# Kernel tuning notes

Measured on AMD Instinct MI355X. Metric: run time of the kernel, lower is better.

## Reference

```python
import jax, jax.numpy as jnp
import numpy as np
from jax import lax

ALPHA = 1.5
N_ITER = 50  # entmax bisect default
GAIN = 1.414


def _p(z):
    # gp_inv(clamp(z,0), alpha) = z_+^(1/(alpha-1)) = z_+^2 for alpha=1.5
    zc = jnp.clip(z, 0.0, None)
    return zc * zc


def entmax15(X):
    """alpha-entmax (alpha=1.5) along last dim via bisection (entmax lib algorithm)."""
    d = X.shape[-1]
    Xs = X * (ALPHA - 1.0)
    mx = jnp.max(Xs, axis=-1, keepdims=True)
    tau_lo = mx - 1.0                       # gp(1, alpha) = 1
    tau_hi = mx - (1.0 / d) ** (ALPHA - 1.0)  # gp(1/d, alpha)
    f_lo = jnp.sum(_p(Xs - tau_lo), axis=-1, keepdims=True) - 1.0

    def body(i, carry):
        tau_lo, dm = carry
        dm = dm * 0.5
        tau_m = tau_lo + dm
        f_m = jnp.sum(_p(Xs - tau_m), axis=-1, keepdims=True) - 1.0
        tau_lo = jnp.where(f_m * f_lo >= 0.0, tau_m, tau_lo)
        return (tau_lo, dm)

    tau_lo, _ = lax.fori_loop(0, N_ITER, body, (tau_lo, tau_hi - tau_lo))
    p = _p(Xs - tau_lo)
    return p / jnp.sum(p, axis=-1, keepdims=True)  # ensure_sum_one=True


def _xavier(key, shape):
    std = GAIN * (2.0 / (shape[0] + shape[1])) ** 0.5
    a = (3.0 ** 0.5) * std
    return jax.random.uniform(key, shape, minval=-a, maxval=a, dtype=jnp.float32)


def setup_inputs() -> dict:
    B, F, E, N = 2048, 64, 256, 64  # batch, nfield, nemb, ncross
    key = jax.random.key(0)
    k1, k2, k3, k4 = jax.random.split(key, 4)
    return {
        "x": jax.random.normal(k1, (B, F, E), dtype=jnp.float32),
        "bilinear_w": _xavier(k2, (E, E)),
        "query": _xavier(k3, (N, E)),
        "value": _xavier(k4, (N, F)),
    }


def reference(x, bilinear_w, query, value):
    # x: [B,F,E]; bilinear_w: [E,E]; query: [N,E]; value: [N,F]
    scale = x.shape[-1] ** -0.5
    k = jnp.einsum('bfe,de->bfd', x, bilinear_w)        # [B,F,E]
    att_gate = jnp.einsum('bfd,nd->bnf', k, query) * scale  # [B,N,F]
    sparse_gate = entmax15(att_gate)                     # entmax over F
    attn_weight = sparse_gate * value[None]              # [B,N,F]
    return jnp.exp(jnp.einsum('bfe,bnf->bne', x, attn_weight))  # [B,N,E]
```

## Files before the change

### kernel.cpp

```cpp
#include <hip/hip_runtime.h>
#include <hip/hip_bf16.h>

typedef __attribute__((ext_vector_type(8))) short bf16x8;
typedef __attribute__((ext_vector_type(4))) float f32x4;

__device__ __forceinline__ unsigned int pk2(float a, float b) {
  union { __hip_bfloat162 h; unsigned int u; } cv;
  cv.h = __float22bfloat162_rn(make_float2(a, b));
  return cv.u;
}
__device__ __forceinline__ unsigned short f2bf(float f) {
  unsigned int u = __float_as_uint(f);
  u += 0x7FFFu + ((u >> 16) & 1u);
  return (unsigned short)(u >> 16);
}

__device__ __forceinline__ float dpp_xor1(float v) {
  return __int_as_float(__builtin_amdgcn_update_dpp(
      0, __float_as_int(v), 0xB1, 0xF, 0xF, true));
}
__device__ __forceinline__ float dpp_xor2(float v) {
  return __int_as_float(__builtin_amdgcn_update_dpp(
      0, __float_as_int(v), 0x4E, 0xF, 0xF, true));
}

__global__ void __launch_bounds__(256) qw_kernel(const float* __restrict__ q,
                                                 const float* __restrict__ W,
                                                 unsigned short* __restrict__ qw) {
  int n = blockIdx.x, e = threadIdx.x;
  float acc = 0.f;
  #pragma unroll 8
  for (int d = 0; d < 256; ++d) acc = fmaf(q[n * 256 + d], W[d * 256 + e], acc);
  qw[n * 256 + e] = f2bf(acc * 0.0625f);
}

__global__ void __launch_bounds__(512, 6) cross_main(
    const float* __restrict__ x, const float* __restrict__ value,
    const unsigned short* __restrict__ qw, float* __restrict__ out) {

  __shared__ __align__(16) unsigned short lds_x[64 * 268];
  __shared__ __align__(16) unsigned char  lds_pool[64 * 68 * 4];

  float* lds_att = (float*)lds_pool;
  unsigned short* lds_aw = (unsigned short*)lds_pool;

  const int t = threadIdx.x;
  const int b = blockIdx.x;
  const int l = t & 63;
  const int w = t >> 6;
  const int l15 = l & 15, l4 = l >> 4;

  {
    const float4* xg = (const float4*)(x + (size_t)b * 16384);
    #pragma unroll
    for (int it = 0; it < 4; ++it) {
      int u = it * 512 + t;
      float4 v0 = xg[2 * u], v1 = xg[2 * u + 1];
      int f = u >> 5, c8 = u & 31;
      char* dst = (char*)lds_x + f * 536 + c8 * 16;
      *(uint2*)dst       = make_uint2(pk2(v0.x, v0.y), pk2(v0.z, v0.w));
      *(uint2*)(dst + 8) = make_uint2(pk2(v1.x, v1.y), pk2(v1.z, v1.w));
    }
  }
  __syncthreads();

  {
    int nt = w >> 1, ft0 = (w & 1) * 2;
    f32x4 acc0 = {0.f, 0.f, 0.f, 0.f}, acc1 = {0.f, 0.f, 0.f, 0.f};
    const unsigned short* qa = qw + (nt * 16 + l15) * 256 + l4 * 8;
    const char* rb0 = (const char*)lds_x + (ft0 * 16 + l15) * 536 + l4 * 16;
    const char* rb1 = rb0 + 16 * 536;
    #pragma unroll
    for (int kc = 0; kc < 8; ++kc) {
      union BF { uint2 d[2]; bf16x8 v; };
      bf16x8 a = *(const bf16x8*)(qa + kc * 32);
      BF b0, b1;
      b0.d[0] = *(const uint2*)(rb0 + kc * 64);
      b0.d[1] = *(const uint2*)(rb0 + kc * 64 + 8);
      b1.d[0] = *(const uint2*)(rb1 + kc * 64);
      b1.d[1] = *(const uint2*)(rb1 + kc * 64 + 8);
      acc0 = __builtin_amdgcn_mfma_f32_16x16x32_bf16(a, b0.v, acc0, 0, 0, 0);
      acc1 = __builtin_amdgcn_mfma_f32_16x16x32_bf16(a, b1.v, acc1, 0, 0, 0);
    }
    int nrow = nt * 16 + 4 * l4;
    #pragma unroll
    for (int r = 0; r < 4; ++r) {
      lds_att[(nrow + r) * 68 + ft0 * 16 + l15]       = acc0[r];
      lds_att[(nrow + r) * 68 + (ft0 + 1) * 16 + l15] = acc1[r];
    }
  }
  __syncthreads();

  {
    int n = w * 8 + (l >> 3);
    int fb = (l & 7) * 8;
    f32x4 z0 = *(const f32x4*)&lds_att[n * 68 + fb];
    f32x4 z1 = *(const f32x4*)&lds_att[n * 68 + fb + 4];
    __syncthreads();
    float z[8];
    #pragma unroll
    for (int k = 0; k < 4; ++k) { z[k] = z0[k] * 0.5f; z[k + 4] = z1[k] * 0.5f; }
    float m = fmaxf(fmaxf(fmaxf(z[0], z[1]), fmaxf(z[2], z[3])),
                    fmaxf(fmaxf(z[4], z[5]), fmaxf(z[6], z[7])));
    m = fmaxf(m, dpp_xor1(m));
    m = fmaxf(m, dpp_xor2(m));
    m = fmaxf(m, __shfl_xor(m, 4));
    float tau = m - 1.0f;
    #pragma unroll
    for (int it = 0; it < 10; ++it) {
      float s0 = 0.f, s1 = 0.f, q0 = 0.f, q1 = 0.f;
      #pragma unroll
      for (int k = 0; k < 4; ++k) {
        float d0 = fmaxf(z[k] - tau, 0.f);
        float d1 = fmaxf(z[k + 4] - tau, 0.f);
        s0 = fmaf(d0, d0, s0); q0 += d0;
        s1 = fmaf(d1, d1, s1); q1 += d1;
      }
      float s = s0 + s1, q = q0 + q1;
      s += dpp_xor1(s); s += dpp_xor2(s); s += __shfl_xor(s, 4);
      q += dpp_xor1(q); q += dpp_xor2(q); q += __shfl_xor(q, 4);
      tau += (s - 1.0f) * 0.5f * __builtin_amdgcn_rcpf(q);
    }
    float p[8]; float S = 0.f;
    #pragma unroll
    for (int k = 0; k < 8; ++k) { float d = fmaxf(z[k] - tau, 0.f); p[k] = d * d; S += p[k]; }
    S += dpp_xor1(S); S += dpp_xor2(S); S += __shfl_xor(S, 4);
    float invS = 1.0f / S;
    const float4* vg = (const float4*)(value + n * 64 + fb);
    float4 va = vg[0], vb = vg[1];
    uint4 pkv;
    pkv.x = pk2(p[0] * invS * va.x, p[1] * invS * va.y);
    pkv.y = pk2(p[2] * invS * va.z, p[3] * invS * va.w);
    pkv.z = pk2(p[4] * invS * vb.x, p[5] * invS * vb.y);
    pkv.w = pk2(p[6] * invS * vb.z, p[7] * invS * vb.w);
    *(uint4*)&lds_aw[n * 72 + fb] = pkv;
  }
  __syncthreads();

  {
    const int te0 = 2 * w;
    f32x4 acc[4][2];
    #pragma unroll
    for (int nt = 0; nt < 4; ++nt) {
      acc[nt][0] = (f32x4){0.f, 0.f, 0.f, 0.f};
      acc[nt][1] = (f32x4){0.f, 0.f, 0.f, 0.f};
    }
    #pragma unroll
    for (int kc = 0; kc < 2; ++kc) {
      bf16x8 a[4];
      #pragma unroll
      for (int nt = 0; nt < 4; ++nt)
        a[nt] = *(const bf16x8*)&lds_aw[(nt * 16 + l15) * 72 + kc * 32 + l4 * 8];
      const char* gp = (const char*)lds_x + (kc * 32 + l4 * 8) * 536 + (te0 * 16 + l15) * 2;
      #pragma unroll
      for (int j = 0; j < 2; ++j) {
        union { unsigned short u[8]; bf16x8 v; } bb;
        #pragma unroll
        for (int i = 0; i < 8; ++i)
          bb.u[i] = *(const unsigned short*)(gp + i * 536 + j * 32);
        #pragma unroll
        for (int nt = 0; nt < 4; ++nt)
          acc[nt][j] = __builtin_amdgcn_mfma_f32_16x16x32_bf16(a[nt], bb.v, acc[nt][j], 0, 0, 0);
      }
    }
    float* ob = out + (size_t)b * 16384;
    #pragma unroll
    for (int nt = 0; nt < 4; ++nt) {
      #pragma unroll
      for (int j = 0; j < 2; ++j) {
        #pragma unroll
        for (int r = 0; r < 4; ++r) {
          ob[(nt * 16 + 4 * l4 + r) * 256 + (te0 + j) * 16 + l15] = __expf(acc[nt][j][r]);
        }
      }
    }
  }
}

extern "C" void kernel_launch(void* const* d_in, const int* in_sizes, int n_in,
                              void* d_out, int out_size, void* d_ws, size_t ws_size,
                              hipStream_t stream) {
  const float* x     = (const float*)d_in[0];
  const float* W     = (const float*)d_in[1];
  const float* q     = (const float*)d_in[2];
  const float* value = (const float*)d_in[3];
  float* out = (float*)d_out;
  unsigned short* qw = (unsigned short*)d_ws;

  qw_kernel<<<dim3(64), dim3(256), 0, stream>>>(q, W, qw);
  cross_main<<<dim3(2048), dim3(512), 0, stream>>>(x, value, qw, out);
}
```

Before: 69.78 us.

## Double block size to 1024 threads, halving per-wave work in every stage

```diff
diff --git a/kernel.cpp b/kernel.cpp
--- a/kernel.cpp
+++ b/kernel.cpp
@@ -34,7 +34,7 @@
   qw[n * 256 + e] = f2bf(acc * 0.0625f);
 }
 
-__global__ void __launch_bounds__(512, 6) cross_main(
+__global__ void __launch_bounds__(1024, 8) cross_main(
     const float* __restrict__ x, const float* __restrict__ value,
     const unsigned short* __restrict__ qw, float* __restrict__ out) {
 
@@ -53,8 +53,8 @@
   {
     const float4* xg = (const float4*)(x + (size_t)b * 16384);
     #pragma unroll
-    for (int it = 0; it < 4; ++it) {
-      int u = it * 512 + t;
+    for (int it = 0; it < 2; ++it) {
+      int u = it * 1024 + t;
       float4 v0 = xg[2 * u], v1 = xg[2 * u + 1];
       int f = u >> 5, c8 = u & 31;
       char* dst = (char*)lds_x + f * 536 + c8 * 16;
@@ -65,115 +65,88 @@
   __syncthreads();
 
   {
-    int nt = w >> 1, ft0 = (w & 1) * 2;
-    f32x4 acc0 = {0.f, 0.f, 0.f, 0.f}, acc1 = {0.f, 0.f, 0.f, 0.f};
+    const int nt = w >> 2, ft = w & 3;
+    f32x4 acc = {0.f, 0.f, 0.f, 0.f};
     const unsigned short* qa = qw + (nt * 16 + l15) * 256 + l4 * 8;
-    const char* rb0 = (const char*)lds_x + (ft0 * 16 + l15) * 536 + l4 * 16;
-    const char* rb1 = rb0 + 16 * 536;
+    const char* rb = (const char*)lds_x + (ft * 16 + l15) * 536 + l4 * 16;
     #pragma unroll
     for (int kc = 0; kc < 8; ++kc) {
-      union BF { uint2 d[2]; bf16x8 v; };
+      union BF { uint2 d[2]; bf16x8 v; } bx;
       bf16x8 a = *(const bf16x8*)(qa + kc * 32);
-      BF b0, b1;
-      b0.d[0] = *(const uint2*)(rb0 + kc * 64);
-      b0.d[1] = *(const uint2*)(rb0 + kc * 64 + 8);
-      b1.d[0] = *(const uint2*)(rb1 + kc * 64);
-      b1.d[1] = *(const uint2*)(rb1 + kc * 64 + 8);
-      acc0 = __builtin_amdgcn_mfma_f32_16x16x32_bf16(a, b0.v, acc0, 0, 0, 0);
-      acc1 = __builtin_amdgcn_mfma_f32_16x16x32_bf16(a, b1.v, acc1, 0, 0, 0);
+      bx.d[0] = *(const uint2*)(rb + kc * 64);
+      bx.d[1] = *(const uint2*)(rb + kc * 64 + 8);
+      acc = __builtin_amdgcn_mfma_f32_16x16x32_bf16(a, bx.v, acc, 0, 0, 0);
     }
     int nrow = nt * 16 + 4 * l4;
     #pragma unroll
-    for (int r = 0; r < 4; ++r) {
-      lds_att[(nrow + r) * 68 + ft0 * 16 + l15]       = acc0[r];
-      lds_att[(nrow + r) * 68 + (ft0 + 1) * 16 + l15] = acc1[r];
-    }
+    for (int r = 0; r < 4; ++r)
+      lds_att[(nrow + r) * 68 + ft * 16 + l15] = acc[r];
   }
   __syncthreads();
 
   {
-    int n = w * 8 + (l >> 3);
-    int fb = (l & 7) * 8;
-    f32x4 z0 = *(const f32x4*)&lds_att[n * 68 + fb];
-    f32x4 z1 = *(const f32x4*)&lds_att[n * 68 + fb + 4];
+    const int n = t >> 4;
+    const int fl = t & 15;
+    f32x4 z4 = *(const f32x4*)&lds_att[n * 68 + fl * 4];
     __syncthreads();
-    float z[8];
+    float z[4];
     #pragma unroll
-    for (int k = 0; k < 4; ++k) { z[k] = z0[k] * 0.5f; z[k + 4] = z1[k] * 0.5f; }
-    float m = fmaxf(fmaxf(fmaxf(z[0], z[1]), fmaxf(z[2], z[3])),
-                    fmaxf(fmaxf(z[4], z[5]), fmaxf(z[6], z[7])));
+    for (int k = 0; k < 4; ++k) z[k] = z4[k] * 0.5f;
+    float m = fmaxf(fmaxf(z[0], z[1]), fmaxf(z[2], z[3]));
     m = fmaxf(m, dpp_xor1(m));
     m = fmaxf(m, dpp_xor2(m));
     m = fmaxf(m, __shfl_xor(m, 4));
+    m = fmaxf(m, __shfl_xor(m, 8));
     float tau = m - 1.0f;
     #pragma unroll
     for (int it = 0; it < 10; ++it) {
-      float s0 = 0.f, s1 = 0.f, q0 = 0.f, q1 = 0.f;
+      float s = 0.f, q = 0.f;
       #pragma unroll
       for (int k = 0; k < 4; ++k) {
-        float d0 = fmaxf(z[k] - tau, 0.f);
-        float d1 = fmaxf(z[k + 4] - tau, 0.f);
-        s0 = fmaf(d0, d0, s0); q0 += d0;
-        s1 = fmaf(d1, d1, s1); q1 += d1;
+        float d = fmaxf(z[k] - tau, 0.f);
+        s = fmaf(d, d, s); q += d;
       }
-      float s = s0 + s1, q = q0 + q1;
-      s += dpp_xor1(s); s += dpp_xor2(s); s += __shfl_xor(s, 4);
-      q += dpp_xor1(q); q += dpp_xor2(q); q += __shfl_xor(q, 4);
+      s += dpp_xor1(s); s += dpp_xor2(s); s += __shfl_xor(s, 4); s += __shfl_xor(s, 8);
+      q += dpp_xor1(q); q += dpp_xor2(q); q += __shfl_xor(q, 4); q += __shfl_xor(q, 8);
       tau += (s - 1.0f) * 0.5f * __builtin_amdgcn_rcpf(q);
     }
-    float p[8]; float S = 0.f;
+    float p[4]; float S = 0.f;
     #pragma unroll
-    for (int k = 0; k < 8; ++k) { float d = fmaxf(z[k] - tau, 0.f); p[k] = d * d; S += p[k]; }
-    S += dpp_xor1(S); S += dpp_xor2(S); S += __shfl_xor(S, 4);
+    for (int k = 0; k < 4; ++k) { float d = fmaxf(z[k] - tau, 0.f); p[k] = d * d; S += p[k]; }
+    S += dpp_xor1(S); S += dpp_xor2(S); S += __shfl_xor(S, 4); S += __shfl_xor(S, 8);
     float invS = 1.0f / S;
-    const float4* vg = (const float4*)(value + n * 64 + fb);
-    float4 va = vg[0], vb = vg[1];
-    uint4 pkv;
-    pkv.x = pk2(p[0] * invS * va.x, p[1] * invS * va.y);
-    pkv.y = pk2(p[2] * invS * va.z, p[3] * invS * va.w);
-    pkv.z = pk2(p[4] * invS * vb.x, p[5] * invS * vb.y);
-    pkv.w = pk2(p[6] * invS * vb.z, p[7] * invS * vb.w);
-    *(uint4*)&lds_aw[n * 72 + fb] = pkv;
+    float4 vv = *(const float4*)(value + n * 64 + fl * 4);
+    uint2 pkd = make_uint2(pk2(p[0] * invS * vv.x, p[1] * invS * vv.y),
+                           pk2(p[2] * invS * vv.z, p[3] * invS * vv.w));
+    *(uint2*)&lds_aw[n * 72 + fl * 4] = pkd;
   }
   __syncthreads();
 
   {
-    const int te0 = 2 * w;
-    f32x4 acc[4][2];
+    f32x4 acc[4];
     #pragma unroll
-    for (int nt = 0; nt < 4; ++nt) {
-      acc[nt][0] = (f32x4){0.f, 0.f, 0.f, 0.f};
-      acc[nt][1] = (f32x4){0.f, 0.f, 0.f, 0.f};
-    }
+    for (int nt2 = 0; nt2 < 4; ++nt2) acc[nt2] = (f32x4){0.f, 0.f, 0.f, 0.f};
     #pragma unroll
     for (int kc = 0; kc < 2; ++kc) {
       bf16x8 a[4];
       #pragma unroll
-      for (int nt = 0; nt < 4; ++nt)
-        a[nt] = *(const bf16x8*)&lds_aw[(nt * 16 + l15) * 72 + kc * 32 + l4 * 8];
-      const char* gp = (const char*)lds_x + (kc * 32 + l4 * 8) * 536 + (te0 * 16 + l15) * 2;
+      for (int nt2 = 0; nt2 < 4; ++nt2)
+        a[nt2] = *(const bf16x8*)&lds_aw[(nt2 * 16 + l15) * 72 + kc * 32 + l4 * 8];
+      const char* gp = (const char*)lds_x + (kc * 32 + l4 * 8) * 536 + (w * 16 + l15) * 2;
+      union { unsigned short u[8]; bf16x8 v; } bb;
       #pragma unroll
-      for (int j = 0; j < 2; ++j) {
-        union { unsigned short u[8]; bf16x8 v; } bb;
-        #pragma unroll
-        for (int i = 0; i < 8; ++i)
-          bb.u[i] = *(const unsigned short*)(gp + i * 536 + j * 32);
-        #pragma unroll
-        for (int nt = 0; nt < 4; ++nt)
-          acc[nt][j] = __builtin_amdgcn_mfma_f32_16x16x32_bf16(a[nt], bb.v, acc[nt][j], 0, 0, 0);
-      }
+      for (int i = 0; i < 8; ++i)
+        bb.u[i] = *(const unsigned short*)(gp + i * 536);
+      #pragma unroll
+      for (int nt2 = 0; nt2 < 4; ++nt2)
+        acc[nt2] = __builtin_amdgcn_mfma_f32_16x16x32_bf16(a[nt2], bb.v, acc[nt2], 0, 0, 0);
     }
     float* ob = out + (size_t)b * 16384;
     #pragma unroll
-    for (int nt = 0; nt < 4; ++nt) {
+    for (int nt2 = 0; nt2 < 4; ++nt2)
       #pragma unroll
-      for (int j = 0; j < 2; ++j) {
-        #pragma unroll
-        for (int r = 0; r < 4; ++r) {
-          ob[(nt * 16 + 4 * l4 + r) * 256 + (te0 + j) * 16 + l15] = __expf(acc[nt][j][r]);
-        }
-      }
-    }
+      for (int r = 0; r < 4; ++r)
+        ob[(nt2 * 16 + 4 * l4 + r) * 256 + w * 16 + l15] = __expf(acc[nt2][r]);
   }
 }
 
@@ -188,5 +161,5 @@
   unsigned short* qw = (unsigned short*)d_ws;
 
   qw_kernel<<<dim3(64), dim3(256), 0, stream>>>(q, W, qw);
-  cross_main<<<dim3(2048), dim3(512), 0, stream>>>(x, value, qw, out);
+  cross_main<<<dim3(2048), dim3(1024), 0, stream>>>(x, value, qw, out);
 }
```

Result: slower. 82.67 us (+18.5%).
